# Performance work log

Measured on AMD Instinct MI355X. Metric: run time of the kernel, lower is better.

## Reference

```python
import jax, jax.numpy as jnp
import numpy as np

NUM_HEADS = 8


def setup_inputs() -> dict:
    key = jax.random.key(0)
    ks = jax.random.split(key, 9)
    B, S, E = 16, 2048, 768
    s = 0.02
    return {
        "features": jax.random.normal(ks[0], (B, S, E), jnp.float32),
        "in_proj_w": jax.random.normal(ks[1], (3 * E, E), jnp.float32) * s,
        "in_proj_b": jnp.zeros((3 * E,), jnp.float32),
        "out_proj_w": jax.random.normal(ks[2], (E, E), jnp.float32) * s,
        "out_proj_b": jnp.zeros((E,), jnp.float32),
        "w1": jax.random.normal(ks[3], (384, E), jnp.float32) * s,
        "b1": jnp.zeros((384,), jnp.float32),
        "w2": jax.random.normal(ks[4], (1, 384), jnp.float32) * s,
        "b2": jnp.zeros((1,), jnp.float32),
    }


def reference(features, in_proj_w, in_proj_b, out_proj_w, out_proj_b, w1, b1, w2, b2):
    # torch nn.MultiheadAttention default batch_first=False: dim 0 is the
    # attended sequence axis (length B here), dim 1 is the MHA batch (S).
    B, S, E = features.shape
    H = NUM_HEADS
    Dh = E // H
    qkv = features @ in_proj_w.T + in_proj_b          # (B, S, 3E)
    q, k, v = jnp.split(qkv, 3, axis=-1)
    q = q.reshape(B, S, H, Dh)
    k = k.reshape(B, S, H, Dh)
    v = v.reshape(B, S, H, Dh)
    scale = 1.0 / jnp.sqrt(jnp.asarray(Dh, features.dtype))
    # attention over axis-0 positions (l, m in 0..B-1), per (s, h)
    scores = jnp.einsum('lshd,mshd->shlm', q * scale, k)
    attn = jax.nn.softmax(scores, axis=-1)
    ctx = jnp.einsum('shlm,mshd->lshd', attn, v).reshape(B, S, E)
    attn_out = ctx @ out_proj_w.T + out_proj_b        # (B, S, E)
    # batched 2-layer MLP (replaces the Python per-row loop)
    h = jax.nn.relu(attn_out @ w1.T + b1)             # (B, S, 384)
    prob = h @ w2.T + b2                              # (B, S, 1)
    contacts = jnp.broadcast_to(prob, (B, S, S))      # contacts[:, i, :] = prob[:, i]
    return contacts
```

## Files before the change

kernel.cpp:

```cpp
#include <hip/hip_runtime.h>

typedef unsigned short u16;
typedef __attribute__((ext_vector_type(8))) __bf16 bf16x8;
typedef __attribute__((ext_vector_type(4))) float floatx4;

#define B_DIM  16
#define S_DIM  2048
#define E_DIM  768
#define HEADS  8
#define DHEAD  96
#define MROWS  32768
#define QKV_LD 2304
#define ATT_ST 392

#define GLDS(gp, lp) __builtin_amdgcn_global_load_lds( \
    (const __attribute__((address_space(1))) void*)(gp), \
    (__attribute__((address_space(3))) void*)(lp), 16, 0, 0)

__device__ __forceinline__ u16 f2b(float f) {
    unsigned u = __float_as_uint(f);
    u += 0x7fffu + ((u >> 16) & 1u);
    return (u16)(u >> 16);
}
__device__ __forceinline__ float blo(unsigned u) { return __uint_as_float(u << 16); }
__device__ __forceinline__ float bhi(unsigned u) { return __uint_as_float(u & 0xffff0000u); }

__device__ __forceinline__ void axpy8(float* acc, float p, uint4 v) {
    acc[0] += p * blo(v.x); acc[1] += p * bhi(v.x);
    acc[2] += p * blo(v.y); acc[3] += p * bhi(v.y);
    acc[4] += p * blo(v.z); acc[5] += p * bhi(v.z);
    acc[6] += p * blo(v.w); acc[7] += p * bhi(v.w);
}

#define PB0 24576
#define PB1 26304
#define PB2 26592
#define PB3 27168
#define PB4 27552
__global__ __launch_bounds__(256) void prep(const float* __restrict__ features,
                                            const float* __restrict__ in_proj_w,
                                            const float* __restrict__ w1,
                                            const float* __restrict__ out_proj_w,
                                            const float* __restrict__ bo,
                                            const float* __restrict__ b1,
                                            u16* __restrict__ fbf, u16* __restrict__ wib,
                                            u16* __restrict__ w1b, u16* __restrict__ WoT,
                                            float* __restrict__ cbuf) {
    __shared__ float tsh[32][33];
    const int b = blockIdx.x, tid = threadIdx.x;
    if (b < PB2) {
        const float* src; u16* dst; long i;
        if (b < PB0)      { src = features;  dst = fbf; i = (long)b * 256 + tid; }
        else if (b < PB1) { src = in_proj_w; dst = wib; i = (long)(b - PB0) * 256 + tid; }
        else              { src = w1;        dst = w1b; i = (long)(b - PB1) * 256 + tid; }
        float4 f = ((const float4*)src)[i];
        ushort4 r;
        r.x = f2b(f.x); r.y = f2b(f.y); r.z = f2b(f.z); r.w = f2b(f.w);
        ((ushort4*)dst)[i] = r;
    } else if (b < PB3) {
        const int t = b - PB2;
        const int bxT = t % 24, byT = t / 24;
        const int tx = tid & 31, ty = tid >> 5;
        int x = bxT * 32 + tx;
        int y = byT * 32 + ty;
#pragma unroll
        for (int j = 0; j < 4; j++) tsh[ty + j * 8][tx] = out_proj_w[(long)(y + j * 8) * 768 + x];
        __syncthreads();
        x = byT * 32 + tx;
        y = bxT * 32 + ty;
#pragma unroll
        for (int j = 0; j < 4; j++) WoT[(long)(y + j * 8) * 768 + x] = f2b(tsh[tx][ty + j * 8]);
    } else {
        const int n = b - PB3;
        const float* row = w1 + (long)n * 768;
        float s = row[tid] * bo[tid] + row[tid + 256] * bo[tid + 256] + row[tid + 512] * bo[tid + 512];
#pragma unroll
        for (int off = 32; off > 0; off >>= 1) s += __shfl_xor(s, off);
        if ((tid & 63) == 0) tsh[0][tid >> 6] = s;
        __syncthreads();
        if (tid == 0) cbuf[n] = tsh[0][0] + tsh[0][1] + tsh[0][2] + tsh[0][3] + b1[n];
    }
}

template<bool PERM, bool SWIZ>
__global__ __launch_bounds__(256) void gemm_bt(const u16* __restrict__ A, int lda,
                                               const u16* __restrict__ W,
                                               const float* __restrict__ bias,
                                               u16* __restrict__ Cout, int ldc,
                                               int N, int K) {
    __shared__ __align__(16) u16 sA[2 * 128 * 32];
    __shared__ __align__(16) u16 sB[2 * 128 * 32];
    __shared__ __align__(16) u16 sC[32 * 132];
    const int tid  = threadIdx.x;
    int bn, bm;
    if (SWIZ) {
        const int bx  = blockIdx.x;
        const int xcd = bx & 7;
        const int q   = bx >> 3;
        const int s   = q / 144;
        const int r   = q % 144;
        bn = r >> 3;
        bm = s * 64 + xcd * 8 + (r & 7);
    } else {
        bn = blockIdx.x;
        bm = blockIdx.y;
    }
    const int lane = tid & 63;
    const int wid  = tid >> 6;
    const int wm   = (wid >> 1) * 64;
    const int wn   = (wid & 1) * 64;
    const int ar = tid >> 2;
    const int ac = (tid & 3) * 8;
    const u16* Ap = A + (long)(bm * 128 + ar) * lda + ac;
    const u16* Wp = W + (long)(bn * 128 + ar) * K + ac;
    const long a2 = (long)64 * lda;
    const long w2 = (long)64 * K;

    floatx4 acc[4][4] = {};
    const int fr = lane & 15;
    const int fq = (lane >> 4) * 8;

    for (int k0 = 0; k0 < K; k0 += 64) {
#pragma unroll
        for (int h = 0; h < 2; h++) {
            GLDS(Ap + k0 + h * 32,      sA + h * 4096 + tid * 8);
            GLDS(Ap + a2 + k0 + h * 32, sA + h * 4096 + 2048 + tid * 8);
            GLDS(Wp + k0 + h * 32,      sB + h * 4096 + tid * 8);
            GLDS(Wp + w2 + k0 + h * 32, sB + h * 4096 + 2048 + tid * 8);
        }
        __syncthreads();
#pragma unroll
        for (int h = 0; h < 2; h++) {
            bf16x8 aF[4], bF[4];
#pragma unroll
            for (int i = 0; i < 4; i++) {
                aF[i] = *(const bf16x8*)(sA + h * 4096 + (wm + i * 16 + fr) * 32 + fq);
                bF[i] = *(const bf16x8*)(sB + h * 4096 + (wn + i * 16 + fr) * 32 + fq);
            }
#pragma unroll
            for (int i = 0; i < 4; i++)
#pragma unroll
                for (int j = 0; j < 4; j++)
                    acc[i][j] = __builtin_amdgcn_mfma_f32_16x16x32_bf16(aF[i], bF[j], acc[i][j], 0, 0, 0);
        }
        __syncthreads();
    }

    const int rq = (lane >> 4) * 4;
    float bvj[4];
#pragma unroll
    for (int j = 0; j < 4; j++)
        bvj[j] = bias ? bias[bn * 128 + wn + j * 16 + fr] : 0.f;
#pragma unroll
    for (int p = 0; p < 4; p++) {
        if ((p >> 1) == (wid >> 1)) {
#pragma unroll
            for (int ii = 0; ii < 2; ii++) {
                const int i = (p & 1) * 2 + ii;
#pragma unroll
                for (int j = 0; j < 4; j++) {
                    const int col = wn + j * 16 + fr;
#pragma unroll
                    for (int r = 0; r < 4; r++)
                        sC[(ii * 16 + rq + r) * 132 + col] = f2b(acc[i][j][r] + bvj[j]);
                }
            }
        }
        __syncthreads();
#pragma unroll
        for (int q2 = 0; q2 < 2; q2++) {
            const int lr = (tid >> 4) + q2 * 16;
            const int c  = tid & 15;
            uint4 v = *(const uint4*)(sC + lr * 132 + c * 8);
            const int rl = bm * 128 + p * 32 + lr;
            const long grow = PERM ? (long)(((rl & 2047) << 4) | (rl >> 11)) : (long)rl;
            *(uint4*)(Cout + grow * ldc + bn * 128 + c * 8) = v;
        }
        __syncthreads();
    }
}

__global__ __launch_bounds__(256) void attn_kernel(u16* __restrict__ qkv) {
    __shared__ __align__(16) u16 sQ[16 * ATT_ST], sK[16 * ATT_ST], sV[16 * ATT_ST];
    __shared__ float sS[4][16][16];
    const int tid = threadIdx.x;
    const int s  = blockIdx.x >> 1;
    const int hh = blockIdx.x & 1;
    const u16* base = qkv + (long)s * 16 * QKV_LD + hh * 384;

#pragma unroll
    for (int it = 0; it < 9; it++) {
        const int i = it * 256 + tid;
        const int t = i / 768, rem = i % 768, l = rem / 48, c = rem % 48;
        const u16* src = base + (long)l * QKV_LD + t * E_DIM + c * 8;
        u16* dst = (t == 0 ? sQ : t == 1 ? sK : sV) + l * ATT_ST + c * 8;
        *(uint4*)dst = *(const uint4*)src;
    }
    __syncthreads();

    const int lane = tid & 63;
    const int w    = tid >> 6;
    const int fr   = lane & 15;
    const int fq   = (lane >> 4) * 8;
    floatx4 acc = {};
    const u16* qrow = sQ + fr * ATT_ST + w * DHEAD + fq;
    const u16* krow = sK + fr * ATT_ST + w * DHEAD + fq;
#pragma unroll
    for (int st = 0; st < 3; st++) {
        bf16x8 qa = *(const bf16x8*)(qrow + st * 32);
        bf16x8 kb = *(const bf16x8*)(krow + st * 32);
        acc = __builtin_amdgcn_mfma_f32_16x16x32_bf16(qa, kb, acc, 0, 0, 0);
    }
    const int rq = (lane >> 4) * 4;
#pragma unroll
    for (int r = 0; r < 4; r++) {
        float sc = acc[r] * 0.10206207261596577f;
        float mx = sc;
#pragma unroll
        for (int off = 8; off > 0; off >>= 1) mx = fmaxf(mx, __shfl_xor(mx, off));
        float e = __expf(sc - mx);
        float sum = e;
#pragma unroll
        for (int off = 8; off > 0; off >>= 1) sum += __shfl_xor(sum, off);
        sS[w][rq + r][fr] = e / sum;
    }
    __syncthreads();

#pragma unroll
    for (int j = 0; j < 3; j++) {
        const int task = j * 256 + tid;
        const int h = task / 192, rem = task % 192, ll = rem / 12, c = rem % 12;
        float a[8] = {};
#pragma unroll
        for (int mm = 0; mm < 16; mm++) {
            const float p = sS[h][ll][mm];
            uint4 vw = *(const uint4*)(sV + mm * ATT_ST + h * DHEAD + c * 8);
            axpy8(a, p, vw);
        }
        ushort4 o0, o1;
        o0.x = f2b(a[0]); o0.y = f2b(a[1]); o0.z = f2b(a[2]); o0.w = f2b(a[3]);
        o1.x = f2b(a[4]); o1.y = f2b(a[5]); o1.z = f2b(a[6]); o1.w = f2b(a[7]);
        u16* dst = qkv + ((long)s * 16 + ll) * QKV_LD + (hh * 4 + h) * DHEAD + c * 8;
        *(ushort4*)dst = o0;
        *(ushort4*)(dst + 4) = o1;
    }
}

__global__ __launch_bounds__(256) void mlp_gemm(const u16* __restrict__ A, int lda,
                                                const u16* __restrict__ G,
                                                const float* __restrict__ cbias,
                                                const float* __restrict__ w2,
                                                float* __restrict__ part) {
    __shared__ __align__(16) u16 sA[2 * 128 * 32];
    __shared__ __align__(16) u16 sB[2 * 128 * 32];
    __shared__ float rowsum[128];
    const int tid = threadIdx.x;
    const int bm  = blockIdx.x / 3;
    const int bn  = blockIdx.x % 3;
    if (tid < 128) rowsum[tid] = 0.f;
    const int lane = tid & 63;
    const int wid  = tid >> 6;
    const int wm   = (wid >> 1) * 64;
    const int wn   = (wid & 1) * 64;
    const int ar = tid >> 2;
    const int ac = (tid & 3) * 8;
    const u16* Ap = A + (long)(bm * 128 + ar) * lda + ac;
    const u16* Wp = G + (long)(bn * 128 + ar) * 768 + ac;
    const long a2 = (long)64 * lda;
    const long w2s = (long)64 * 768;
    const int fr = lane & 15;
    const int fq = (lane >> 4) * 8;
    const int rq = (lane >> 4) * 4;

    floatx4 acc[4][4] = {};
    for (int k0 = 0; k0 < 768; k0 += 64) {
#pragma unroll
        for (int h = 0; h < 2; h++) {
            GLDS(Ap + k0 + h * 32,       sA + h * 4096 + tid * 8);
            GLDS(Ap + a2 + k0 + h * 32,  sA + h * 4096 + 2048 + tid * 8);
            GLDS(Wp + k0 + h * 32,       sB + h * 4096 + tid * 8);
            GLDS(Wp + w2s + k0 + h * 32, sB + h * 4096 + 2048 + tid * 8);
        }
        __syncthreads();
#pragma unroll
        for (int h = 0; h < 2; h++) {
            bf16x8 aF[4], bF[4];
#pragma unroll
            for (int i = 0; i < 4; i++) {
                aF[i] = *(const bf16x8*)(sA + h * 4096 + (wm + i * 16 + fr) * 32 + fq);
                bF[i] = *(const bf16x8*)(sB + h * 4096 + (wn + i * 16 + fr) * 32 + fq);
            }
#pragma unroll
            for (int i = 0; i < 4; i++)
#pragma unroll
                for (int j = 0; j < 4; j++)
                    acc[i][j] = __builtin_amdgcn_mfma_f32_16x16x32_bf16(aF[i], bF[j], acc[i][j], 0, 0, 0);
        }
        __syncthreads();
    }
    float partl[4][4] = {};
#pragma unroll
    for (int j = 0; j < 4; j++) {
        const int col = bn * 128 + wn + j * 16 + fr;
        const float cv = cbias[col];
        const float wv = w2[col];
#pragma unroll
        for (int i = 0; i < 4; i++)
#pragma unroll
            for (int r = 0; r < 4; r++)
                partl[i][r] += fmaxf(acc[i][j][r] + cv, 0.f) * wv;
    }
#pragma unroll
    for (int i = 0; i < 4; i++)
#pragma unroll
        for (int r = 0; r < 4; r++) {
            float v = partl[i][r];
#pragma unroll
            for (int off = 8; off > 0; off >>= 1) v += __shfl_xor(v, off);
            if (fr == 0) atomicAdd(&rowsum[wm + i * 16 + rq + r], v);
        }
    __syncthreads();
    if (tid < 128) part[(long)bn * MROWS + bm * 128 + tid] = rowsum[tid];
}

__global__ __launch_bounds__(256) void bcast_kernel(const float* __restrict__ part,
                                                    const float* __restrict__ b2,
                                                    float* __restrict__ out) {
    const int tid = threadIdx.x;
    const long s  = blockIdx.x;
    const float b2v = b2[0];
#pragma unroll
    for (int l = 0; l < 16; l++) {
        const long p = s * 16 + l;
        const float pv = part[p] + part[MROWS + p] + part[2 * MROWS + p] + b2v;
        floatx4 v4 = {pv, pv, pv, pv};
        floatx4* dst = (floatx4*)(out + ((long)l * S_DIM + s) * S_DIM);
        __builtin_nontemporal_store(v4, dst + tid);
        __builtin_nontemporal_store(v4, dst + tid + 256);
    }
}

extern "C" void kernel_launch(void* const* d_in, const int* in_sizes, int n_in,
                              void* d_out, int out_size, void* d_ws, size_t ws_size,
                              hipStream_t stream) {
    const float* features   = (const float*)d_in[0];
    const float* in_proj_b  = (const float*)d_in[2];
    const float* out_proj_b = (const float*)d_in[4];
    const float* b1 = (const float*)d_in[6];
    const float* w2 = (const float*)d_in[7];
    const float* b2 = (const float*)d_in[8];
    float* out = (float*)d_out;

    char* p = (char*)d_ws;
    u16* fbf = (u16*)p; p += (size_t)MROWS * E_DIM * 2;
    u16* wib = (u16*)p; p += (size_t)QKV_LD * E_DIM * 2;
    u16* w1b = (u16*)p; p += (size_t)384 * E_DIM * 2;
    u16* WoT = (u16*)p; p += (size_t)E_DIM * E_DIM * 2;
    u16* Gbf = (u16*)p; p += (size_t)384 * E_DIM * 2;
    float* cbuf  = (float*)p; p += 384 * 4;
    float* partb = (float*)p; p += (size_t)3 * MROWS * 4;
    p = (char*)(((size_t)p + 255) & ~(size_t)255);
    u16* qkv = (u16*)p; p += (size_t)MROWS * QKV_LD * 2;
    u16* ctx = qkv;

    prep<<<PB4, 256, 0, stream>>>(features, (const float*)d_in[1], (const float*)d_in[5],
                                  (const float*)d_in[3], out_proj_b, b1,
                                  fbf, wib, w1b, WoT, cbuf);
    gemm_bt<false, false><<<dim3(6, 3), 256, 0, stream>>>(
        w1b, E_DIM, WoT, nullptr, Gbf, E_DIM, E_DIM, E_DIM);
    gemm_bt<true, true><<<dim3(4608), 256, 0, stream>>>(
        fbf, E_DIM, wib, in_proj_b, qkv, QKV_LD, QKV_LD, E_DIM);
    attn_kernel<<<S_DIM * 2, 256, 0, stream>>>(qkv);
    mlp_gemm<<<768, 256, 0, stream>>>(ctx, QKV_LD, Gbf, cbuf, w2, partb);
    bcast_kernel<<<S_DIM, 256, 0, stream>>>(partb, b2, out);
}
```

Before: 591.5 us.

## Merge small G GEMM into QKV GEMM launch and XCD-swizzle attention and MLP blocks

Folds the small 18-block w1×WoT GEMM into the QKV projection kernel as extra leading blocks, removing one kernel launch and its tail. It also remaps block indices in the attention and MLP GEMM kernels so that consecutive rows handled by the same XCD share L2 locality. The fused kernel now uses runtime selection of operands and the perm flag instead of template parameters, which may add some register and branch overhead.

New measurement: 579.9 us. -2.0%, faster.

```diff
diff --git a/kernel.cpp b/kernel.cpp
--- a/kernel.cpp
+++ b/kernel.cpp
@@ -82,28 +82,34 @@
     }
 }
 
-template<bool PERM, bool SWIZ>
-__global__ __launch_bounds__(256) void gemm_bt(const u16* __restrict__ A, int lda,
-                                               const u16* __restrict__ W,
-                                               const float* __restrict__ bias,
-                                               u16* __restrict__ Cout, int ldc,
-                                               int N, int K) {
+__global__ __launch_bounds__(256) void qkv_g_kernel(const u16* __restrict__ A, int lda,
+                                                    const u16* __restrict__ W,
+                                                    const float* __restrict__ bias,
+                                                    u16* __restrict__ Cout, int ldc, int K,
+                                                    const u16* __restrict__ gA,
+                                                    const u16* __restrict__ gW,
+                                                    u16* __restrict__ gC) {
     __shared__ __align__(16) u16 sA[2 * 128 * 32];
     __shared__ __align__(16) u16 sB[2 * 128 * 32];
     __shared__ __align__(16) u16 sC[32 * 132];
-    const int tid  = threadIdx.x;
-    int bn, bm;
-    if (SWIZ) {
-        const int bx  = blockIdx.x;
-        const int xcd = bx & 7;
-        const int q   = bx >> 3;
+    const int tid = threadIdx.x;
+    const int bx  = blockIdx.x;
+    int bn, bm, lda_, ldc_, K_;
+    const u16 *Aa, *Ww; const float* bs; u16* Co; bool perm;
+    if (bx < 18) {
+        bn = bx % 6; bm = bx / 6;
+        Aa = gA; Ww = gW; bs = nullptr; Co = gC;
+        lda_ = 768; ldc_ = 768; K_ = 768; perm = false;
+    } else {
+        const int b2  = bx - 18;
+        const int xcd = b2 & 7;
+        const int q   = b2 >> 3;
         const int s   = q / 144;
         const int r   = q % 144;
         bn = r >> 3;
         bm = s * 64 + xcd * 8 + (r & 7);
-    } else {
-        bn = blockIdx.x;
-        bm = blockIdx.y;
+        Aa = A; Ww = W; bs = bias; Co = Cout;
+        lda_ = lda; ldc_ = ldc; K_ = K; perm = true;
     }
     const int lane = tid & 63;
     const int wid  = tid >> 6;
@@ -111,16 +117,16 @@
     const int wn   = (wid & 1) * 64;
     const int ar = tid >> 2;
     const int ac = (tid & 3) * 8;
-    const u16* Ap = A + (long)(bm * 128 + ar) * lda + ac;
-    const u16* Wp = W + (long)(bn * 128 + ar) * K + ac;
-    const long a2 = (long)64 * lda;
-    const long w2 = (long)64 * K;
+    const u16* Ap = Aa + (long)(bm * 128 + ar) * lda_ + ac;
+    const u16* Wp = Ww + (long)(bn * 128 + ar) * K_ + ac;
+    const long a2 = (long)64 * lda_;
+    const long w2 = (long)64 * K_;
 
     floatx4 acc[4][4] = {};
     const int fr = lane & 15;
     const int fq = (lane >> 4) * 8;
 
-    for (int k0 = 0; k0 < K; k0 += 64) {
+    for (int k0 = 0; k0 < K_; k0 += 64) {
 #pragma unroll
         for (int h = 0; h < 2; h++) {
             GLDS(Ap + k0 + h * 32,      sA + h * 4096 + tid * 8);
@@ -150,7 +156,7 @@
     float bvj[4];
 #pragma unroll
     for (int j = 0; j < 4; j++)
-        bvj[j] = bias ? bias[bn * 128 + wn + j * 16 + fr] : 0.f;
+        bvj[j] = bs ? bs[bn * 128 + wn + j * 16 + fr] : 0.f;
 #pragma unroll
     for (int p = 0; p < 4; p++) {
         if ((p >> 1) == (wid >> 1)) {
@@ -173,8 +179,8 @@
             const int c  = tid & 15;
             uint4 v = *(const uint4*)(sC + lr * 132 + c * 8);
             const int rl = bm * 128 + p * 32 + lr;
-            const long grow = PERM ? (long)(((rl & 2047) << 4) | (rl >> 11)) : (long)rl;
-            *(uint4*)(Cout + grow * ldc + bn * 128 + c * 8) = v;
+            const long grow = perm ? (long)(((rl & 2047) << 4) | (rl >> 11)) : (long)rl;
+            *(uint4*)(Co + grow * ldc_ + bn * 128 + c * 8) = v;
         }
         __syncthreads();
     }
@@ -184,8 +190,13 @@
     __shared__ __align__(16) u16 sQ[16 * ATT_ST], sK[16 * ATT_ST], sV[16 * ATT_ST];
     __shared__ float sS[4][16][16];
     const int tid = threadIdx.x;
-    const int s  = blockIdx.x >> 1;
-    const int hh = blockIdx.x & 1;
+    const int bx  = blockIdx.x;
+    const int xcd   = bx & 7;
+    const int rest  = bx >> 3;
+    const int hh    = rest & 1;
+    const int inner = (rest >> 1) & 63;
+    const int outer = rest >> 7;
+    const int s = (outer << 9) | (xcd << 6) | inner;
     const u16* base = qkv + (long)s * 16 * QKV_LD + hh * 384;
 
 #pragma unroll
@@ -255,8 +266,12 @@
     __shared__ __align__(16) u16 sB[2 * 128 * 32];
     __shared__ float rowsum[128];
     const int tid = threadIdx.x;
-    const int bm  = blockIdx.x / 3;
-    const int bn  = blockIdx.x % 3;
+    const int bx  = blockIdx.x;
+    const int xcd = bx & 7;
+    const int q   = bx >> 3;
+    const int bn  = q % 3;
+    const int t   = q / 3;
+    const int bm  = ((t >> 3) << 6) | (xcd << 3) | (t & 7);
     if (tid < 128) rowsum[tid] = 0.f;
     const int lane = tid & 63;
     const int wid  = tid >> 6;
@@ -366,10 +381,8 @@
     prep<<<PB4, 256, 0, stream>>>(features, (const float*)d_in[1], (const float*)d_in[5],
                                   (const float*)d_in[3], out_proj_b, b1,
                                   fbf, wib, w1b, WoT, cbuf);
-    gemm_bt<false, false><<<dim3(6, 3), 256, 0, stream>>>(
-        w1b, E_DIM, WoT, nullptr, Gbf, E_DIM, E_DIM, E_DIM);
-    gemm_bt<true, true><<<dim3(4608), 256, 0, stream>>>(
-        fbf, E_DIM, wib, in_proj_b, qkv, QKV_LD, QKV_LD, E_DIM);
+    qkv_g_kernel<<<4626, 256, 0, stream>>>(fbf, E_DIM, wib, in_proj_b, qkv, QKV_LD, E_DIM,
+                                           w1b, WoT, Gbf);
     attn_kernel<<<S_DIM * 2, 256, 0, stream>>>(qkv);
     mlp_gemm<<<768, 256, 0, stream>>>(ctx, QKV_LD, Gbf, cbuf, w2, partb);
     bcast_kernel<<<S_DIM, 256, 0, stream>>>(partb, b2, out);
```
